# Kernel optimization log

Hardware: AMD Instinct MI355X
Metric: run time of the kernel (lower is better)

The kernel has to match this reference:

```python
import jax, jax.numpy as jnp
import numpy as np

B, S, D, L, H = 8, 1024, 512, 6, 8
HD = D // H


def setup_inputs() -> dict:
    key = jax.random.key(0)
    sc = D ** -0.5
    inp = {
        "xr": jax.random.normal(jax.random.fold_in(key, 0), (B, S, D), jnp.float32),
        "xi": jax.random.normal(jax.random.fold_in(key, 1), (B, S, D), jnp.float32),
    }
    wnames = ["Wq_r", "Wq_i", "Wk_r", "Wk_i", "Wv_r", "Wv_i", "Wo_r", "Wo_i",
              "W1_r", "W1_i", "W2_r", "W2_i"]
    for i, n in enumerate(wnames):
        inp[n] = jax.random.normal(jax.random.fold_in(key, 10 + i), (L, D, D), jnp.float32) * sc
    for n in ["bq_r", "bq_i", "bk_r", "bk_i", "bv_r", "bv_i", "bo_r", "bo_i",
              "b1_r", "b1_i", "b2_r", "b2_i"]:
        inp[n] = jnp.zeros((L, D), jnp.float32)
    g0 = 1.0 / np.sqrt(2.0)  # standard complex-LN affine init
    for n in ["ln1_grr", "ln1_gii", "ln2_grr", "ln2_gii"]:
        inp[n] = jnp.full((L, D), g0, jnp.float32)
    for n in ["ln1_gri", "ln1_br", "ln1_bi", "ln2_gri", "ln2_br", "ln2_bi"]:
        inp[n] = jnp.zeros((L, D), jnp.float32)
    return inp


def clin(xr, xi, Wr, Wi, br, bi):
    # ComplexLinear: (xr + i xi)(Wr + i Wi)^T + (br + i bi)
    yr = xr @ Wr.T - xi @ Wi.T + br
    yi = xr @ Wi.T + xi @ Wr.T + bi
    return yr, yi


def cln(xr, xi, grr, gri, gii, br, bi, eps=1e-5):
    # Complex LayerNorm: 2x2 covariance whitening over the feature dim + affine
    mr = xr.mean(-1, keepdims=True)
    mi = xi.mean(-1, keepdims=True)
    cr, ci = xr - mr, xi - mi
    Vrr = (cr * cr).mean(-1, keepdims=True) + eps
    Vii = (ci * ci).mean(-1, keepdims=True) + eps
    Vri = (cr * ci).mean(-1, keepdims=True)
    s = jnp.sqrt(Vrr * Vii - Vri * Vri)
    t = jnp.sqrt(Vrr + Vii + 2.0 * s)
    st = s * t
    Wrr = (Vii + s) / st
    Wii = (Vrr + s) / st
    Wri = -Vri / st
    hr = Wrr * cr + Wri * ci
    hi = Wri * cr + Wii * ci
    return grr * hr + gri * hi + br, gri * hr + gii * hi + bi


def reference(xr, xi,
              Wq_r, Wq_i, bq_r, bq_i, Wk_r, Wk_i, bk_r, bk_i,
              Wv_r, Wv_i, bv_r, bv_i, Wo_r, Wo_i, bo_r, bo_i,
              W1_r, W1_i, b1_r, b1_i, W2_r, W2_i, b2_r, b2_i,
              ln1_grr, ln1_gri, ln1_gii, ln1_br, ln1_bi,
              ln2_grr, ln2_gri, ln2_gii, ln2_br, ln2_bi):
    b, s, d = xr.shape
    nl = Wq_r.shape[0]
    h = H
    hd = d // h
    scale = hd ** -0.5
    for l in range(nl):
        rr, ri = xr, xi
        qr, qi = clin(xr, xi, Wq_r[l], Wq_i[l], bq_r[l], bq_i[l])
        kr, ki = clin(xr, xi, Wk_r[l], Wk_i[l], bk_r[l], bk_i[l])
        vr, vi = clin(xr, xi, Wv_r[l], Wv_i[l], bv_r[l], bv_i[l])
        split = lambda a: a.reshape(b, s, h, hd)
        qr, qi, kr, ki, vr, vi = map(split, (qr, qi, kr, ki, vr, vi))
        # sm_variante='real': softmax over Re(q k^H) = qr.kr + qi.ki
        logits = (jnp.einsum('bqhd,bkhd->bhqk', qr, kr)
                  + jnp.einsum('bqhd,bkhd->bhqk', qi, ki)) * scale
        A = jax.nn.softmax(logits, axis=-1)  # real-valued attention weights
        o_r = jnp.einsum('bhqk,bkhd->bqhd', A, vr).reshape(b, s, d)
        o_i = jnp.einsum('bhqk,bkhd->bqhd', A, vi).reshape(b, s, d)
        o_r, o_i = clin(o_r, o_i, Wo_r[l], Wo_i[l], bo_r[l], bo_i[l])
        xr, xi = o_r + rr, o_i + ri
        xr, xi = cln(xr, xi, ln1_grr[l], ln1_gri[l], ln1_gii[l], ln1_br[l], ln1_bi[l])
        rr, ri = xr, xi
        hr, hi = clin(xr, xi, W1_r[l], W1_i[l], b1_r[l], b1_i[l])
        hr, hi = jax.nn.relu(hr), jax.nn.relu(hi)  # CReLU; dropout = identity (eval)
        hr, hi = clin(hr, hi, W2_r[l], W2_i[l], b2_r[l], b2_i[l])
        xr, xi = hr + rr, hi + ri
        xr, xi = cln(xr, xi, ln2_grr[l], ln2_gri[l], ln2_gii[l], ln2_br[l], ln2_bi[l])
    return jnp.stack([xr, xi])  # [2, B, S, D] (real, imag)
```

## Files before the change

kernel.cpp:

```cpp
#include <hip/hip_runtime.h>
#include <cstddef>
#include <cstdint>

constexpr int NB   = 8;
constexpr int SEQ  = 1024;
constexpr int DIM  = 512;
constexpr int NL   = 6;
constexpr int NH   = 8;
constexpr int HDIM = 64;
constexpr int ROWS = NB * SEQ;
constexpr size_t BSD = (size_t)ROWS * DIM;
constexpr int KHAT = 1024;

typedef __attribute__((ext_vector_type(8))) short bfrag;
typedef __attribute__((ext_vector_type(4))) float f32x4;
typedef __attribute__((ext_vector_type(4))) unsigned short us4;

__device__ __forceinline__ void f4a(const float4 v, float* a) {
    a[0] = v.x; a[1] = v.y; a[2] = v.z; a[3] = v.w;
}
__device__ __forceinline__ float4 a4f(const float* a) {
    float4 v; v.x = a[0]; v.y = a[1]; v.z = a[2]; v.w = a[3]; return v;
}
__device__ __forceinline__ unsigned short f2bf(float f) {
    union { float f; uint32_t u; } x{f};
    return (unsigned short)((x.u + 0x7fffu + ((x.u >> 16) & 1u)) >> 16);
}
__device__ __forceinline__ float bf2f(unsigned short u) {
    union { uint32_t u; float f; } x;
    x.u = (uint32_t)u << 16;
    return x.f;
}
__device__ __forceinline__ uint32_t cvtpk(float lo, float hi) {
    uint32_t r;
    asm("v_cvt_pk_bf16_f32 %0, %1, %2" : "=v"(r) : "v"(lo), "v"(hi));
    return r;
}
__device__ __forceinline__ void gload16(const unsigned short* g, void* l) {
    __builtin_amdgcn_global_load_lds(
        (const __attribute__((address_space(1))) void*)g,
        (__attribute__((address_space(3))) void*)l, 16, 0, 0);
}

constexpr float ATT_SC = 0.125f * 1.44269504f;

struct PrepArgs {
    const float* Wr[6]; const float* Wi[6];
    const float* br[6]; const float* bi[6];
};

__global__ __launch_bounds__(256)
void prep_kernel(PrepArgs a, unsigned short* __restrict__ Ball,
                 float* __restrict__ biasall, int layer)
{
    const int lin = blockIdx.y;
    const int nh_ = blockIdx.x;
    const float* Wr = a.Wr[lin] + (size_t)layer * DIM * DIM;
    const float* Wi = a.Wi[lin] + (size_t)layer * DIM * DIM;

    bool real; int n0;
    if (lin < 3) { const int dh = nh_ & 127; real = dh < 64; n0 = (nh_ >> 7) * 64 + (dh & 63); }
    else         { real = nh_ < 512; n0 = nh_ & 511; }

    const int t = threadIdx.x;
    const int kk = (t * 4) & 511;
    const bool fh = t < 128;
    const float* src;
    float sgn = 1.f;
    if (fh) src = real ? Wr : Wi;
    else { if (real) { src = Wi; sgn = -1.f; } else src = Wr; }

    float v[4];
    f4a(*(const float4*)(src + (size_t)n0 * 512 + kk), v);
    us4 o;
    #pragma unroll
    for (int j = 0; j < 4; ++j) o[j] = f2bf(sgn * v[j]);
    *(us4*)(Ball + (size_t)lin * KHAT * KHAT + (size_t)nh_ * KHAT + t * 4) = o;
    if (t == 0)
        biasall[lin * KHAT + nh_] = real ? a.br[lin][layer * DIM + n0]
                                         : a.bi[lin][layer * DIM + n0];
}

__global__ __launch_bounds__(256)
void gemm_qkv(const unsigned short* __restrict__ Xh,
              const unsigned short* __restrict__ Ball,
              const float* __restrict__ biasall,
              unsigned short* __restrict__ Qh,
              unsigned short* __restrict__ Kh,
              unsigned short* __restrict__ Vth)
{
    __shared__ __align__(16) unsigned short Asm[2][128 * 32];
    __shared__ __align__(16) unsigned short Bsm[2][128 * 32];

    const int t = threadIdx.x, lane = t & 63, w = t >> 6;
    const int wm = w >> 1, wn = w & 1;
    const int c = lane & 15, g = lane >> 4;

    int bid = blockIdx.y * 24 + blockIdx.x;
    bid = (bid & 7) * 192 + (bid >> 3);
    const int nblk = bid % 24, mblk = bid / 24;
    const int n0g = nblk * 128;
    const int m0 = mblk * 128;
    const int lin = n0g >> 10;
    const int n0 = n0g & 1023;
    const unsigned short* Bh = Ball + (size_t)lin * KHAT * KHAT;
    const float* bias = biasall + lin * KHAT;

    f32x4 acc[4][4];
    #pragma unroll
    for (int i = 0; i < 4; ++i)
        #pragma unroll
        for (int j = 0; j < 4; ++j) acc[i][j] = (f32x4){0.f, 0.f, 0.f, 0.f};

    const int srow = (w << 4) + (lane >> 2);
    const int scol = (lane & 3) * 8;
    const unsigned short* gA0 = Xh + (size_t)(m0 + srow) * KHAT + scol;
    const unsigned short* gA1 = Xh + (size_t)(m0 + 64 + srow) * KHAT + scol;
    const unsigned short* gB0 = Bh + (size_t)(n0 + srow) * KHAT + scol;
    const unsigned short* gB1 = Bh + (size_t)(n0 + 64 + srow) * KHAT + scol;
    char* aB0 = (char*)Asm[0] + (w << 10);
    char* aB1 = (char*)Asm[1] + (w << 10);
    char* bB0 = (char*)Bsm[0] + (w << 10);
    char* bB1 = (char*)Bsm[1] + (w << 10);

    for (int ks = 0; ks < 16; ++ks) {
        const int k0 = ks * 64;
        __syncthreads();
        gload16(gA0 + k0, aB0);
        gload16(gA1 + k0, aB0 + 4096);
        gload16(gB0 + k0, bB0);
        gload16(gB1 + k0, bB0 + 4096);
        gload16(gA0 + k0 + 32, aB1);
        gload16(gA1 + k0 + 32, aB1 + 4096);
        gload16(gB0 + k0 + 32, bB1);
        gload16(gB1 + k0 + 32, bB1 + 4096);
        __syncthreads();

        #pragma unroll
        for (int h = 0; h < 2; ++h) {
            bfrag af[4], bf2[4];
            #pragma unroll
            for (int mi = 0; mi < 4; ++mi)
                af[mi] = *(const bfrag*)(Asm[h] + (wm * 64 + mi * 16 + c) * 32 + g * 8);
            #pragma unroll
            for (int ni = 0; ni < 4; ++ni)
                bf2[ni] = *(const bfrag*)(Bsm[h] + (wn * 64 + ni * 16 + c) * 32 + g * 8);
            #pragma unroll
            for (int mi = 0; mi < 4; ++mi)
                #pragma unroll
                for (int ni = 0; ni < 4; ++ni)
                    acc[mi][ni] = __builtin_amdgcn_mfma_f32_16x16x32_bf16(
                        af[mi], bf2[ni], acc[mi][ni], 0, 0, 0);
        }
    }

    const int mbase = m0 + wm * 64;
    const int nbase = n0 + wn * 64;
    unsigned short* dqk = (lin == 0) ? Qh : Kh;
    #pragma unroll
    for (int mi = 0; mi < 4; ++mi) {
        #pragma unroll
        for (int ni = 0; ni < 4; ++ni) {
            const int n = nbase + ni * 16 + c;
            const float bv = bias[n];
            float v[4];
            #pragma unroll
            for (int r = 0; r < 4; ++r) {
                v[r] = acc[mi][ni][r] + bv;
                if (lin == 0) v[r] *= ATT_SC;
            }
            const int mrow = mbase + mi * 16 + g * 4;
            const int b = mrow >> 10, s = mrow & 1023;
            const int h = n >> 7, dh = n & 127;
            if (lin < 2) {
                const size_t a = ((size_t)(b * NH + h) * SEQ + s) * 128 + dh;
                #pragma unroll
                for (int r = 0; r < 4; ++r) dqk[a + (size_t)r * 128] = f2bf(v[r]);
            } else {
                const int ck = (s & 31) >> 2;
                const int sp = (s & ~31) | ((((ck & 3) << 1) | (ck >> 2)) << 2);
                const size_t a = ((size_t)(b * NH + h) * 128 + dh) * SEQ + sp;
                us4 o;
                #pragma unroll
                for (int r = 0; r < 4; ++r) o[r] = f2bf(v[r]);
                *(us4*)(Vth + a) = o;
            }
        }
    }
}

template <bool RELU>
__global__ __launch_bounds__(256)
void gemm_mfma(const unsigned short* __restrict__ Xh,
               const unsigned short* __restrict__ Bh,
               const float* __restrict__ bias,
               unsigned short* __restrict__ Yh)
{
    __shared__ __align__(16) unsigned short Asm[2][128 * 32];
    __shared__ __align__(16) unsigned short Bsm[2][128 * 32];

    const int t = threadIdx.x, lane = t & 63, w = t >> 6;
    const int wm = w >> 1, wn = w & 1;
    const int c = lane & 15, g = lane >> 4;

    int bid = blockIdx.y * 8 + blockIdx.x;
    bid = (bid & 7) * 64 + (bid >> 3);
    const int n0 = (bid & 7) * 128;
    const int m0 = (bid >> 3) * 128;

    f32x4 acc[4][4];
    #pragma unroll
    for (int i = 0; i < 4; ++i)
        #pragma unroll
        for (int j = 0; j < 4; ++j) acc[i][j] = (f32x4){0.f, 0.f, 0.f, 0.f};

    const int srow = (w << 4) + (lane >> 2);
    const int scol = (lane & 3) * 8;
    const unsigned short* gA0 = Xh + (size_t)(m0 + srow) * KHAT + scol;
    const unsigned short* gA1 = Xh + (size_t)(m0 + 64 + srow) * KHAT + scol;
    const unsigned short* gB0 = Bh + (size_t)(n0 + srow) * KHAT + scol;
    const unsigned short* gB1 = Bh + (size_t)(n0 + 64 + srow) * KHAT + scol;
    char* aB0 = (char*)Asm[0] + (w << 10);
    char* aB1 = (char*)Asm[1] + (w << 10);
    char* bB0 = (char*)Bsm[0] + (w << 10);
    char* bB1 = (char*)Bsm[1] + (w << 10);

    for (int ks = 0; ks < 16; ++ks) {
        const int k0 = ks * 64;
        __syncthreads();
        gload16(gA0 + k0, aB0);
        gload16(gA1 + k0, aB0 + 4096);
        gload16(gB0 + k0, bB0);
        gload16(gB1 + k0, bB0 + 4096);
        gload16(gA0 + k0 + 32, aB1);
        gload16(gA1 + k0 + 32, aB1 + 4096);
        gload16(gB0 + k0 + 32, bB1);
        gload16(gB1 + k0 + 32, bB1 + 4096);
        __syncthreads();

        #pragma unroll
        for (int h = 0; h < 2; ++h) {
            bfrag af[4], bf2[4];
            #pragma unroll
            for (int mi = 0; mi < 4; ++mi)
                af[mi] = *(const bfrag*)(Asm[h] + (wm * 64 + mi * 16 + c) * 32 + g * 8);
            #pragma unroll
            for (int ni = 0; ni < 4; ++ni)
                bf2[ni] = *(const bfrag*)(Bsm[h] + (wn * 64 + ni * 16 + c) * 32 + g * 8);
            #pragma unroll
            for (int mi = 0; mi < 4; ++mi)
                #pragma unroll
                for (int ni = 0; ni < 4; ++ni)
                    acc[mi][ni] = __builtin_amdgcn_mfma_f32_16x16x32_bf16(
                        af[mi], bf2[ni], acc[mi][ni], 0, 0, 0);
        }
    }

    const int mbase = m0 + wm * 64;
    const int nbase = n0 + wn * 64;
    #pragma unroll
    for (int mi = 0; mi < 4; ++mi) {
        #pragma unroll
        for (int ni = 0; ni < 4; ++ni) {
            const int n = nbase + ni * 16 + c;
            const float bv = bias[n];
            const int mrow = mbase + mi * 16 + g * 4;
            #pragma unroll
            for (int r = 0; r < 4; ++r) {
                float v = acc[mi][ni][r] + bv;
                if (RELU) v = fmaxf(v, 0.f);
                Yh[(size_t)(mrow + r) * KHAT + n] = f2bf(v);
            }
        }
    }
}

__global__ __launch_bounds__(256)
void attn_mfma(const unsigned short* __restrict__ Qh,
               const unsigned short* __restrict__ Kh,
               const unsigned short* __restrict__ Vth,
               unsigned short* __restrict__ Ah)
{
    __shared__ __align__(16) char smem[32768];
    char* Ksm = smem;
    char* Vsm = smem + 16384;
    const int t    = threadIdx.x;
    const int lane = t & 63;
    const int wv   = t >> 6;
    const int c    = lane & 15;
    const int g    = lane >> 4;

    int bid = blockIdx.x + 8 * blockIdx.y + 64 * blockIdx.z;
    bid = (bid & 7) * 64 + (bid >> 3);
    const int q0 = (bid & 7) * 128;
    const int bh = bid >> 3;
    const int hh = bh & 7, bb = bh >> 3;
    const size_t qkb = (size_t)bh * SEQ * 128;
    const size_t vtb = (size_t)bh * 128 * SEQ;

    constexpr float THR = 11.0f;

    bfrag qf[2][4];
    #pragma unroll
    for (int u = 0; u < 2; ++u) {
        const unsigned short* qp = Qh + qkb + (size_t)(q0 + wv * 32 + u * 16 + c) * 128 + g * 8;
        #pragma unroll
        for (int ks = 0; ks < 4; ++ks) qf[u][ks] = *(const bfrag*)(qp + ks * 32);
    }

    f32x4 oacc[2][8];
    #pragma unroll
    for (int u = 0; u < 2; ++u)
        #pragma unroll
        for (int i = 0; i < 8; ++i) oacc[u][i] = (f32x4){0.f, 0.f, 0.f, 0.f};
    float mrun[2] = {-1e30f, -1e30f}, lrun[2] = {0.f, 0.f};

    const int kkey = t >> 2, kq = t & 3;
    const unsigned short* kgp = Kh + qkb + (size_t)kkey * 128 + kq * 32;
    const int vd = t >> 1, vh2 = t & 1;
    const unsigned short* vgp = Vth + vtb + (size_t)vd * SEQ + vh2 * 32;

    bfrag krg[4], vrg[4];
    #pragma unroll
    for (int j = 0; j < 4; ++j) krg[j] = *(const bfrag*)(kgp + j * 8);
    #pragma unroll
    for (int j = 0; j < 4; ++j) vrg[j] = *(const bfrag*)(vgp + j * 8);

    for (int k0 = 0; k0 < SEQ; k0 += 64) {
        __syncthreads();
        #pragma unroll
        for (int j = 0; j < 4; ++j) {
            const int boff = (kkey * 256 + (kq * 32 + j * 8) * 2) ^ ((kkey & 7) << 4);
            *(bfrag*)(Ksm + boff) = krg[j];
        }
        #pragma unroll
        for (int j = 0; j < 4; ++j) {
            const int boff = (vd * 128 + (vh2 * 32 + j * 8) * 2) ^ ((vd & 7) << 4);
            *(bfrag*)(Vsm + boff) = vrg[j];
        }
        __syncthreads();

        if (k0 + 64 < SEQ) {
            const int kn = k0 + 64;
            #pragma unroll
            for (int j = 0; j < 4; ++j) krg[j] = *(const bfrag*)(kgp + (size_t)kn * 128 + j * 8);
            #pragma unroll
            for (int j = 0; j < 4; ++j) vrg[j] = *(const bfrag*)(vgp + kn + j * 8);
        }

        f32x4 sa[2][4];
        #pragma unroll
        for (int u = 0; u < 2; ++u)
            #pragma unroll
            for (int nt = 0; nt < 4; ++nt) sa[u][nt] = (f32x4){0.f, 0.f, 0.f, 0.f};
        __builtin_amdgcn_s_setprio(1);
        #pragma unroll
        for (int nt = 0; nt < 4; ++nt) {
            const int key = nt * 16 + c;
            bfrag kf[4];
            #pragma unroll
            for (int ks = 0; ks < 4; ++ks) {
                const int boff = (key * 256 + (ks * 32 + g * 8) * 2) ^ ((key & 7) << 4);
                kf[ks] = *(const bfrag*)(Ksm + boff);
            }
            #pragma unroll
            for (int u = 0; u < 2; ++u)
                #pragma unroll
                for (int ks = 0; ks < 4; ++ks)
                    sa[u][nt] = __builtin_amdgcn_mfma_f32_16x16x32_bf16(kf[ks], qf[u][ks], sa[u][nt], 0, 0, 0);
        }
        __builtin_amdgcn_s_setprio(0);

        uint32_t pk0[2][4], pk1[2][4];
        #pragma unroll
        for (int u = 0; u < 2; ++u) {
            float mloc = sa[u][0][0];
            #pragma unroll
            for (int nt = 0; nt < 4; ++nt)
                #pragma unroll
                for (int r = 0; r < 4; ++r) mloc = fmaxf(mloc, sa[u][nt][r]);
            if (__any(mloc > mrun[u] + THR)) {
                float mt = mloc;
                mt = fmaxf(mt, __shfl_xor(mt, 16, 64));
                mt = fmaxf(mt, __shfl_xor(mt, 32, 64));
                const float mn = fmaxf(mrun[u], mt);
                const float fs = exp2f(mrun[u] - mn);
                mrun[u] = mn;
                lrun[u] *= fs;
                #pragma unroll
                for (int i = 0; i < 8; ++i) {
                    oacc[u][i][0] *= fs; oacc[u][i][1] *= fs;
                    oacc[u][i][2] *= fs; oacc[u][i][3] *= fs;
                }
            }
            float ps = 0.f;
            #pragma unroll
            for (int nt = 0; nt < 4; ++nt) {
                float p0 = exp2f(sa[u][nt][0] - mrun[u]);
                float p1 = exp2f(sa[u][nt][1] - mrun[u]);
                float p2 = exp2f(sa[u][nt][2] - mrun[u]);
                float p3 = exp2f(sa[u][nt][3] - mrun[u]);
                ps += (p0 + p1) + (p2 + p3);
                pk0[u][nt] = cvtpk(p0, p1);
                pk1[u][nt] = cvtpk(p2, p3);
            }
            ps += __shfl_xor(ps, 16, 64);
            ps += __shfl_xor(ps, 32, 64);
            lrun[u] += ps;
        }

        __builtin_amdgcn_s_setprio(1);
        #pragma unroll
        for (int k2 = 0; k2 < 2; ++k2) {
            union { uint32_t u[4]; bfrag f; } pb0, pb1;
            pb0.u[0] = pk0[0][2 * k2]; pb0.u[1] = pk1[0][2 * k2];
            pb0.u[2] = pk0[0][2 * k2 + 1]; pb0.u[3] = pk1[0][2 * k2 + 1];
            pb1.u[0] = pk0[1][2 * k2]; pb1.u[1] = pk1[1][2 * k2];
            pb1.u[2] = pk0[1][2 * k2 + 1]; pb1.u[3] = pk1[1][2 * k2 + 1];
            const int kb2 = (k2 * 32 + g * 8) * 2;
            #pragma unroll
            for (int mtl = 0; mtl < 8; ++mtl) {
                const int d = mtl * 16 + c;
                const bfrag va = *(const bfrag*)(Vsm + ((d * 128 + kb2) ^ ((d & 7) << 4)));
                oacc[0][mtl] = __builtin_amdgcn_mfma_f32_16x16x32_bf16(va, pb0.f, oacc[0][mtl], 0, 0, 0);
                oacc[1][mtl] = __builtin_amdgcn_mfma_f32_16x16x32_bf16(va, pb1.f, oacc[1][mtl], 0, 0, 0);
            }
        }
        __builtin_amdgcn_s_setprio(0);
    }

    #pragma unroll
    for (int u = 0; u < 2; ++u) {
        const float ic = 1.0f / lrun[u];
        #pragma unroll
        for (int i = 0; i < 8; ++i) {
            oacc[u][i][0] *= ic; oacc[u][i][1] *= ic;
            oacc[u][i][2] *= ic; oacc[u][i][3] *= ic;
        }
    }
    __syncthreads();
    float* Ox = (float*)(smem + wv * 8192);
    const int q = lane >> 2, qt = lane & 3;
    const int colbase = (qt >> 1) * 512 + hh * 64 + (qt & 1) * 32;
    #pragma unroll
    for (int u = 0; u < 2; ++u) {
        #pragma unroll
        for (int mtl = 0; mtl < 8; ++mtl)
            #pragma unroll
            for (int r = 0; r < 4; ++r)
                Ox[(mtl * 16 + 4 * g + r) * 16 + c] = oacc[u][mtl][r];
        asm volatile("s_waitcnt lgkmcnt(0)" ::: "memory");
        __builtin_amdgcn_sched_barrier(0);

        const size_t rowm = (size_t)bb * SEQ + q0 + wv * 32 + u * 16 + q;
        unsigned short* dst = Ah + rowm * KHAT + colbase;
        #pragma unroll
        for (int j = 0; j < 8; ++j) {
            us4 o;
            #pragma unroll
            for (int e = 0; e < 4; ++e) o[e] = f2bf(Ox[(qt * 32 + j * 4 + e) * 16 + q]);
            *(us4*)(dst + j * 4) = o;
        }
        asm volatile("s_waitcnt lgkmcnt(0)" ::: "memory");
        __builtin_amdgcn_sched_barrier(0);
    }
}

__global__ __launch_bounds__(256)
void cln_kernel(const unsigned short* __restrict__ U,
                float* __restrict__ Xr, float* __restrict__ Xi,
                unsigned short* __restrict__ Xh,
                const float* __restrict__ Grr, const float* __restrict__ Gri,
                const float* __restrict__ Gii, const float* __restrict__ Bbr,
                const float* __restrict__ Bbi)
{
    const int lane = threadIdx.x & 63;
    const int row  = blockIdx.x * 4 + (threadIdx.x >> 6);
    const size_t off = (size_t)row * DIM;
    const int c0 = lane * 4;
    const int c1 = 256 + lane * 4;

    float xr[8], xi[8];
    {
        const unsigned short* up = U + (size_t)row * KHAT;
        us4 a0 = *(const us4*)(up + c0);
        us4 a1 = *(const us4*)(up + c1);
        us4 b0 = *(const us4*)(up + 512 + c0);
        us4 b1 = *(const us4*)(up + 512 + c1);
        float t0[4], t1[4];
        f4a(*(const float4*)&Xr[off + c0], t0);
        f4a(*(const float4*)&Xr[off + c1], t1);
        #pragma unroll
        for (int j = 0; j < 4; ++j) { xr[j] = bf2f(a0[j]) + t0[j]; xr[4 + j] = bf2f(a1[j]) + t1[j]; }
        f4a(*(const float4*)&Xi[off + c0], t0);
        f4a(*(const float4*)&Xi[off + c1], t1);
        #pragma unroll
        for (int j = 0; j < 4; ++j) { xi[j] = bf2f(b0[j]) + t0[j]; xi[4 + j] = bf2f(b1[j]) + t1[j]; }
    }

    float sr = 0.f, si = 0.f, srr = 0.f, sii = 0.f, sri = 0.f;
    #pragma unroll
    for (int j = 0; j < 8; ++j) {
        sr += xr[j]; si += xi[j];
        srr = fmaf(xr[j], xr[j], srr);
        sii = fmaf(xi[j], xi[j], sii);
        sri = fmaf(xr[j], xi[j], sri);
    }
    #pragma unroll
    for (int m = 32; m >= 1; m >>= 1) {
        sr  += __shfl_xor(sr,  m, 64);
        si  += __shfl_xor(si,  m, 64);
        srr += __shfl_xor(srr, m, 64);
        sii += __shfl_xor(sii, m, 64);
        sri += __shfl_xor(sri, m, 64);
    }

    const float inv_d = 1.0f / DIM;
    const float mr = sr * inv_d, mi = si * inv_d;
    const float Vrr = srr * inv_d - mr * mr + 1e-5f;
    const float Vii = sii * inv_d - mi * mi + 1e-5f;
    const float Vri = sri * inv_d - mr * mi;
    const float s  = sqrtf(Vrr * Vii - Vri * Vri);
    const float tt = sqrtf(Vrr + Vii + 2.0f * s);
    const float ist = 1.0f / (s * tt);
    const float Wrr = (Vii + s) * ist;
    const float Wii = (Vrr + s) * ist;
    const float Wri = -Vri * ist;

    #pragma unroll
    for (int half = 0; half < 2; ++half) {
        const int c = half ? c1 : c0;
        float grr[4], gri[4], gii[4], pbr[4], pbi[4];
        f4a(*(const float4*)&Grr[c], grr);
        f4a(*(const float4*)&Gri[c], gri);
        f4a(*(const float4*)&Gii[c], gii);
        f4a(*(const float4*)&Bbr[c], pbr);
        f4a(*(const float4*)&Bbi[c], pbi);
        float outr[4], outi[4];
        #pragma unroll
        for (int j = 0; j < 4; ++j) {
            const int idx = half * 4 + j;
            const float cr = xr[idx] - mr;
            const float ci = xi[idx] - mi;
            const float hr = Wrr * cr + Wri * ci;
            const float hi = Wri * cr + Wii * ci;
            outr[j] = fmaf(grr[j], hr, fmaf(gri[j], hi, pbr[j]));
            outi[j] = fmaf(gri[j], hr, fmaf(gii[j], hi, pbi[j]));
        }
        *(float4*)&Xr[off + c] = a4f(outr);
        *(float4*)&Xi[off + c] = a4f(outi);
        us4 hr_, hi_;
        #pragma unroll
        for (int j = 0; j < 4; ++j) { hr_[j] = f2bf(outr[j]); hi_[j] = f2bf(outi[j]); }
        *(us4*)(Xh + (size_t)row * KHAT + c)       = hr_;
        *(us4*)(Xh + (size_t)row * KHAT + 512 + c) = hi_;
    }
}

__global__ __launch_bounds__(256)
void init_cvt(const float* __restrict__ xr, const float* __restrict__ xi,
              float* __restrict__ outr, float* __restrict__ outi,
              unsigned short* __restrict__ Xh)
{
    const size_t i = ((size_t)blockIdx.x * 256 + threadIdx.x) * 4;
    float vr[4], vi[4];
    f4a(*(const float4*)(xr + i), vr);
    f4a(*(const float4*)(xi + i), vi);
    *(float4*)(outr + i) = a4f(vr);
    *(float4*)(outi + i) = a4f(vi);
    const size_t m = i >> 9;
    const int k = (int)(i & 511);
    us4 a, b;
    #pragma unroll
    for (int j = 0; j < 4; ++j) { a[j] = f2bf(vr[j]); b[j] = f2bf(vi[j]); }
    *(us4*)(Xh + m * KHAT + k)       = a;
    *(us4*)(Xh + m * KHAT + 512 + k) = b;
}

extern "C" void kernel_launch(void* const* d_in, const int* in_sizes, int n_in,
                              void* d_out, int out_size, void* d_ws, size_t ws_size,
                              hipStream_t stream) {
    (void)in_sizes; (void)n_in; (void)out_size; (void)ws_size;

    const float* in_xr = (const float*)d_in[0];
    const float* in_xi = (const float*)d_in[1];
    PrepArgs pa;
    pa.Wr[0] = (const float*)d_in[2];  pa.Wi[0] = (const float*)d_in[3];
    pa.Wr[1] = (const float*)d_in[4];  pa.Wi[1] = (const float*)d_in[5];
    pa.Wr[2] = (const float*)d_in[6];  pa.Wi[2] = (const float*)d_in[7];
    pa.Wr[3] = (const float*)d_in[8];  pa.Wi[3] = (const float*)d_in[9];
    pa.Wr[4] = (const float*)d_in[10]; pa.Wi[4] = (const float*)d_in[11];
    pa.Wr[5] = (const float*)d_in[12]; pa.Wi[5] = (const float*)d_in[13];
    pa.br[0] = (const float*)d_in[14]; pa.bi[0] = (const float*)d_in[15];
    pa.br[1] = (const float*)d_in[16]; pa.bi[1] = (const float*)d_in[17];
    pa.br[2] = (const float*)d_in[18]; pa.bi[2] = (const float*)d_in[19];
    pa.br[3] = (const float*)d_in[20]; pa.bi[3] = (const float*)d_in[21];
    pa.br[4] = (const float*)d_in[22]; pa.bi[4] = (const float*)d_in[23];
    pa.br[5] = (const float*)d_in[24]; pa.bi[5] = (const float*)d_in[25];
    const float* ln1_grr = (const float*)d_in[26];
    const float* ln1_gii = (const float*)d_in[27];
    const float* ln2_grr = (const float*)d_in[28];
    const float* ln2_gii = (const float*)d_in[29];
    const float* ln1_gri = (const float*)d_in[30];
    const float* ln1_br  = (const float*)d_in[31];
    const float* ln1_bi  = (const float*)d_in[32];
    const float* ln2_gri = (const float*)d_in[33];
    const float* ln2_br  = (const float*)d_in[34];
    const float* ln2_bi  = (const float*)d_in[35];

    float* outr = (float*)d_out;
    float* outi = outr + BSD;

    char* ws = (char*)d_ws;
    unsigned short* Xh  = (unsigned short*)(ws);
    unsigned short* Qh  = (unsigned short*)(ws + 16777216);
    unsigned short* Kh  = (unsigned short*)(ws + 2 * 16777216);
    unsigned short* Vth = (unsigned short*)(ws + 3 * 16777216);
    unsigned short* Ah  = (unsigned short*)(ws + 4 * 16777216);
    unsigned short* Ball = (unsigned short*)(ws + 5 * 16777216);
    float* biasall = (float*)(ws + 5 * 16777216 + 12582912);
    unsigned short* Uh = Kh;
    unsigned short* Hh = Qh;

    init_cvt<<<ROWS * DIM / 1024, 256, 0, stream>>>(in_xr, in_xi, outr, outi, Xh);

    const dim3 pgrid(KHAT, 6);
    const dim3 qgrid(24, ROWS / 128);
    const dim3 ggrid(KHAT / 128, ROWS / 128);
    const dim3 agrid(SEQ / 128, NH, NB);
    const int  lgrid = ROWS / 4;

    for (int l = 0; l < NL; ++l) {
        const size_t bo = (size_t)l * DIM;
        prep_kernel<<<pgrid, 256, 0, stream>>>(pa, Ball, biasall, l);

        unsigned short* Bo = Ball + (size_t)3 * KHAT * KHAT;
        unsigned short* B1 = Ball + (size_t)4 * KHAT * KHAT;
        unsigned short* B2 = Ball + (size_t)5 * KHAT * KHAT;

        gemm_qkv<<<qgrid, 256, 0, stream>>>(Xh, Ball, biasall, Qh, Kh, Vth);
        attn_mfma<<<agrid, 256, 0, stream>>>(Qh, Kh, Vth, Ah);
        gemm_mfma<false><<<ggrid, 256, 0, stream>>>(Ah, Bo, biasall + 3 * KHAT, Uh);
        cln_kernel<<<lgrid, 256, 0, stream>>>(Uh, outr, outi, Xh,
                                              ln1_grr + bo, ln1_gri + bo, ln1_gii + bo,
                                              ln1_br + bo, ln1_bi + bo);
        gemm_mfma<true><<<ggrid, 256, 0, stream>>>(Xh, B1, biasall + 4 * KHAT, Hh);
        gemm_mfma<false><<<ggrid, 256, 0, stream>>>(Hh, B2, biasall + 5 * KHAT, Uh);
        cln_kernel<<<lgrid, 256, 0, stream>>>(Uh, outr, outi, Xh,
                                              ln2_grr + bo, ln2_gri + bo, ln2_gii + bo,
                                              ln2_br + bo, ln2_bi + bo);
    }
}
```

Baseline: 1.498 ms.

## Double-buffer K/V tiles in LDS to drop one barrier per attention iteration

Shared memory for the attention kernel doubles to 64KB so K/V tiles can ping-pong between two LDS buffers. The next tile is written into the alternate buffer after the compute, which leaves one __syncthreads per iteration instead of two. Swizzled LDS offsets are precomputed once. The larger LDS footprint may lower the number of resident blocks per CU and reduce latency hiding.

```diff
diff --git a/kernel.cpp b/kernel.cpp
--- a/kernel.cpp
+++ b/kernel.cpp
@@ -281,9 +281,7 @@
                const unsigned short* __restrict__ Vth,
                unsigned short* __restrict__ Ah)
 {
-    __shared__ __align__(16) char smem[32768];
-    char* Ksm = smem;
-    char* Vsm = smem + 16384;
+    __shared__ __align__(16) char smem[65536];
     const int t    = threadIdx.x;
     const int lane = t & 63;
     const int wv   = t >> 6;
@@ -320,28 +318,40 @@
     const int vd = t >> 1, vh2 = t & 1;
     const unsigned short* vgp = Vth + vtb + (size_t)vd * SEQ + vh2 * 32;
 
+    const int kboff[4] = {
+        (kkey * 256 + (kq * 32 + 0 * 8) * 2) ^ ((kkey & 7) << 4),
+        (kkey * 256 + (kq * 32 + 1 * 8) * 2) ^ ((kkey & 7) << 4),
+        (kkey * 256 + (kq * 32 + 2 * 8) * 2) ^ ((kkey & 7) << 4),
+        (kkey * 256 + (kq * 32 + 3 * 8) * 2) ^ ((kkey & 7) << 4)};
+    const int vboff[4] = {
+        (vd * 128 + (vh2 * 32 + 0 * 8) * 2) ^ ((vd & 7) << 4),
+        (vd * 128 + (vh2 * 32 + 1 * 8) * 2) ^ ((vd & 7) << 4),
+        (vd * 128 + (vh2 * 32 + 2 * 8) * 2) ^ ((vd & 7) << 4),
+        (vd * 128 + (vh2 * 32 + 3 * 8) * 2) ^ ((vd & 7) << 4)};
+
     bfrag krg[4], vrg[4];
     #pragma unroll
     for (int j = 0; j < 4; ++j) krg[j] = *(const bfrag*)(kgp + j * 8);
     #pragma unroll
     for (int j = 0; j < 4; ++j) vrg[j] = *(const bfrag*)(vgp + j * 8);
-
-    for (int k0 = 0; k0 < SEQ; k0 += 64) {
-        __syncthreads();
-        #pragma unroll
-        for (int j = 0; j < 4; ++j) {
-            const int boff = (kkey * 256 + (kq * 32 + j * 8) * 2) ^ ((kkey & 7) << 4);
-            *(bfrag*)(Ksm + boff) = krg[j];
-        }
-        #pragma unroll
-        for (int j = 0; j < 4; ++j) {
-            const int boff = (vd * 128 + (vh2 * 32 + j * 8) * 2) ^ ((vd & 7) << 4);
-            *(bfrag*)(Vsm + boff) = vrg[j];
-        }
-        __syncthreads();
-
-        if (k0 + 64 < SEQ) {
-            const int kn = k0 + 64;
+    {
+        char* Kw = smem;
+        char* Vw = smem + 16384;
+        #pragma unroll
+        for (int j = 0; j < 4; ++j) *(bfrag*)(Kw + kboff[j]) = krg[j];
+        #pragma unroll
+        for (int j = 0; j < 4; ++j) *(bfrag*)(Vw + vboff[j]) = vrg[j];
+    }
+    __syncthreads();
+
+    for (int tix = 0; tix < SEQ / 64; ++tix) {
+        const int p = tix & 1;
+        char* Ksm = smem + p * 32768;
+        char* Vsm = Ksm + 16384;
+        const bool more = (tix + 1) < SEQ / 64;
+
+        if (more) {
+            const int kn = (tix + 1) * 64;
             #pragma unroll
             for (int j = 0; j < 4; ++j) krg[j] = *(const bfrag*)(kgp + (size_t)kn * 128 + j * 8);
             #pragma unroll
@@ -427,6 +437,16 @@
             }
         }
         __builtin_amdgcn_s_setprio(0);
+
+        if (more) {
+            char* Kw = smem + (p ^ 1) * 32768;
+            char* Vw = Kw + 16384;
+            #pragma unroll
+            for (int j = 0; j < 4; ++j) *(bfrag*)(Kw + kboff[j]) = krg[j];
+            #pragma unroll
+            for (int j = 0; j < 4; ++j) *(bfrag*)(Vw + vboff[j]) = vrg[j];
+        }
+        __syncthreads();
     }
 
     #pragma unroll
```

New measurement: 1.493 ms. Within noise of the previous version (-0.4%).
